# Kernel optimization log

Hardware: AMD Instinct MI355X
Metric: run time of the kernel (lower is better)

## Reference

```python
import jax, jax.numpy as jnp
import numpy as np

N, E = 20000, 160000
F, H, OUT = 256, 8, 128
L = 6            # total layers -> 5 GAT layers
LM1 = L - 1
NGN = L // 3 + 1 # 3 GraphNorms
D = F // H       # 32 per head
GN_FREQ = 3
EPS = 1e-5


def setup_inputs() -> dict:
    key = jax.random.key(0)
    ks = jax.random.split(key, 12)
    x = jax.random.normal(ks[0], (N, 1), dtype=jnp.float32)
    edge_index = jax.random.randint(ks[1], (2, E), 0, N, dtype=jnp.int32)
    W0 = jax.random.normal(ks[2], (1, F), dtype=jnp.float32) * 0.1
    b0 = jnp.zeros((F,), jnp.float32)
    gat_lin = jax.random.normal(ks[3], (LM1, F, F), dtype=jnp.float32) * (1.0 / np.sqrt(F))
    att_src = jax.random.normal(ks[4], (LM1, H, D), dtype=jnp.float32) * 0.1
    att_dst = jax.random.normal(ks[5], (LM1, H, D), dtype=jnp.float32) * 0.1
    gat_bias = jnp.zeros((LM1, F), jnp.float32)
    gn_weight = jnp.ones((NGN, F), jnp.float32)
    gn_bias = jnp.zeros((NGN, F), jnp.float32)
    gn_mean_scale = jnp.ones((NGN, F), jnp.float32)
    lin_W = jax.random.normal(ks[6], (F, OUT), dtype=jnp.float32) * (1.0 / np.sqrt(F))
    lin_b = jnp.zeros((OUT,), jnp.float32)
    return {"x": x, "W0": W0, "b0": b0, "gat_lin": gat_lin, "att_src": att_src,
            "att_dst": att_dst, "gat_bias": gat_bias, "gn_weight": gn_weight,
            "gn_bias": gn_bias, "gn_mean_scale": gn_mean_scale,
            "lin_W": lin_W, "lin_b": lin_b, "edge_index": edge_index}


def _gcn_conv(x, W, b, src, dst, n):
    h = x @ W
    deg = jax.ops.segment_sum(jnp.ones(src.shape[0], h.dtype), dst, num_segments=n)
    dinv = jnp.where(deg > 0, jax.lax.rsqrt(deg), 0.0)
    norm = dinv[src] * dinv[dst]                      # [E']
    out = jax.ops.segment_sum(h[src] * norm[:, None], dst, num_segments=n)
    return out + b


def _gat_conv(x, W, a_src, a_dst, src, dst, n):
    # PyG GATConv (concat=True, negative_slope=0.2, self-loops in src/dst)
    h = (x @ W).reshape(n, H, D)
    s = jnp.einsum('nhd,hd->nh', h, a_src)            # [N,H]
    t = jnp.einsum('nhd,hd->nh', h, a_dst)
    e = jax.nn.leaky_relu(s[src] + t[dst], 0.2)       # [E',H]
    m = jax.ops.segment_max(e, dst, num_segments=n)   # per-dst softmax
    e = jnp.exp(e - m[dst])
    denom = jax.ops.segment_sum(e, dst, num_segments=n)
    alpha = e / (denom[dst] + 1e-16)
    out = jax.ops.segment_sum(h[src] * alpha[:, :, None], dst, num_segments=n)
    return out.reshape(n, F)


def _graph_norm(x, w, b, ms):
    # PyG GraphNorm with batch=None (single graph): per-feature stats over nodes
    mean = jnp.mean(x, axis=0)
    out = x - ms * mean
    var = jnp.mean(out * out, axis=0)
    return w * out * jax.lax.rsqrt(var + EPS) + b


def reference(x, W0, b0, gat_lin, att_src, att_dst, gat_bias, gn_weight, gn_bias,
              gn_mean_scale, lin_W, lin_b, edge_index):
    n = x.shape[0]
    loops = jnp.arange(n, dtype=edge_index.dtype)
    src = jnp.concatenate([edge_index[0], loops])
    dst = jnp.concatenate([edge_index[1], loops])
    h = jax.nn.relu(_gcn_conv(x, W0, b0, src, dst, n))
    for i in range(LM1):
        if i % GN_FREQ == 0:
            g = i // GN_FREQ
            h = _graph_norm(h, gn_weight[g], gn_bias[g], gn_mean_scale[g])
        out = _gat_conv(h, gat_lin[i], att_src[i], att_dst[i], src, dst, n)
        if i % GN_FREQ == 0:
            out = out + gat_bias[i]
        h = h + jax.nn.relu(out)
    return h @ lin_W + lin_b
```

## Files before the change

### kernel.cpp

```cpp
#include <hip/hip_runtime.h>
#include <hip/hip_bf16.h>
#include <stdint.h>

typedef float f32x4 __attribute__((ext_vector_type(4)));
typedef short s16x8 __attribute__((ext_vector_type(8)));

__device__ __forceinline__ float bf2f(unsigned short u) {
    union { unsigned int i; float f; } v; v.i = ((unsigned int)u) << 16; return v.f;
}
__device__ __forceinline__ unsigned short f2bf(float f) {
    union { float f; unsigned int i; } v; v.f = f;
    unsigned int x = v.i;
    return (unsigned short)((x + 0x7fffu + ((x >> 16) & 1u)) >> 16);
}
__device__ __forceinline__ void gload16(const void* g, void* l) {
    __builtin_amdgcn_global_load_lds(
        (const __attribute__((address_space(1))) void*)g,
        (__attribute__((address_space(3))) void*)l, 16, 0, 0);
}

__global__ void k_init_deg(int* deg, int n) {
    int i = blockIdx.x * blockDim.x + threadIdx.x;
    if (i < n) deg[i] = 1;
}

__global__ void k_count(const int* __restrict__ ei, int E, int* deg) {
    int e = blockIdx.x * blockDim.x + threadIdx.x;
    if (e < E) atomicAdd(&deg[ei[E + e]], 1);
}

__global__ __launch_bounds__(256) void k_bsum(const int* __restrict__ deg,
                                              int* __restrict__ bsum, int n) {
    __shared__ int buf[256];
    int i = blockIdx.x * 256 + threadIdx.x;
    buf[threadIdx.x] = (i < n) ? deg[i] : 0;
    __syncthreads();
#pragma unroll
    for (int off = 128; off > 0; off >>= 1) {
        if ((int)threadIdx.x < off) buf[threadIdx.x] += buf[threadIdx.x + off];
        __syncthreads();
    }
    if (threadIdx.x == 0) bsum[blockIdx.x] = buf[0];
}

__global__ __launch_bounds__(256) void k_scanb(const int* __restrict__ bsum,
                                               int* __restrict__ boff, int nb) {
    __shared__ int buf[256];
    int t = threadIdx.x;
    int v = (t < nb) ? bsum[t] : 0;
    buf[t] = v;
    __syncthreads();
    for (int off = 1; off < 256; off <<= 1) {
        int add = (t >= off) ? buf[t - off] : 0;
        __syncthreads();
        buf[t] += add;
        __syncthreads();
    }
    if (t < nb) boff[t] = buf[t] - v;
}

__global__ __launch_bounds__(256) void k_emit(const int* __restrict__ deg,
                                              const int* __restrict__ boff,
                                              int* __restrict__ rowptr,
                                              int* __restrict__ wo,
                                              float* __restrict__ dinv, int n) {
    __shared__ int buf[256];
    int i = blockIdx.x * 256 + threadIdx.x;
    int v = (i < n) ? deg[i] : 0;
    buf[threadIdx.x] = v;
    __syncthreads();
    for (int off = 1; off < 256; off <<= 1) {
        int add = ((int)threadIdx.x >= off) ? buf[threadIdx.x - off] : 0;
        __syncthreads();
        buf[threadIdx.x] += add;
        __syncthreads();
    }
    if (i < n) {
        int excl = boff[blockIdx.x] + buf[threadIdx.x] - v;
        rowptr[i] = excl;
        wo[i] = excl;
        dinv[i] = rsqrtf((float)v);
        if (i == n - 1) rowptr[n] = excl + v;
    }
}

__global__ void k_fill(const int* __restrict__ ei, int E, int n,
                       int* wo, int* srcs) {
    int e = blockIdx.x * blockDim.x + threadIdx.x;
    int EP = E + n;
    if (e >= EP) return;
    int s_, d_;
    if (e < E) { s_ = ei[e]; d_ = ei[E + e]; }
    else       { s_ = d_ = e - E; }
    int pos = atomicAdd(&wo[d_], 1);
    srcs[pos] = s_;
}

__global__ __launch_bounds__(256) void k_h0f(const float* __restrict__ x,
                                             const float* __restrict__ dinv,
                                             const int* __restrict__ rowptr,
                                             const int* __restrict__ srcs,
                                             const float* __restrict__ W0,
                                             const float* __restrict__ b0,
                                             unsigned short* __restrict__ hbf, int n) {
    int node = blockIdx.x;
    int tid = threadIdx.x;
    if (node >= n) { hbf[(size_t)node * 256 + tid] = 0; return; }
    __shared__ float sv;
    if (tid < 64) {
        int p0 = rowptr[node], p1 = rowptr[node + 1];
        float sum = 0.f;
        for (int p = p0 + tid; p < p1; p += 64) {
            int s = srcs[p];
            sum += x[s] * dinv[s];
        }
#pragma unroll
        for (int m = 1; m < 64; m <<= 1) sum += __shfl_xor(sum, m);
        if (tid == 0) sv = sum * dinv[node];
    }
    __syncthreads();
    float v = fmaxf(sv * W0[tid] + b0[tid], 0.f);
    hbf[(size_t)node * 256 + tid] = f2bf(v);
}

__global__ void k_wprep(const float* __restrict__ gat_lin,
                        const float* __restrict__ lin_W,
                        const float* __restrict__ att_src,
                        const float* __restrict__ att_dst,
                        unsigned short* __restrict__ Wt,
                        unsigned short* __restrict__ lt) {
    int idx = blockIdx.x * blockDim.x + threadIdx.x;
    const int T1 = 5 * 65536;
    const int T2 = T1 + 128 * 256;
    const int T3 = T2 + 5 * 64 * 256;
    if (idx < T1) {
        int l = idx >> 16, r = idx & 0xFFFF;
        int nrow = r >> 8, k = r & 255;
        Wt[(size_t)l * 81920 + nrow * 256 + k] =
            f2bf(gat_lin[(size_t)l * 65536 + k * 256 + nrow]);
    } else if (idx < T2) {
        int j = idx - T1;
        int nrow = j >> 8, k = j & 255;
        lt[nrow * 256 + k] = f2bf(lin_W[(size_t)k * 128 + nrow]);
    } else if (idx < T3) {
        int j = idx - T2;
        int l = j >> 14, r = j & 16383;
        int row = r >> 8, k = r & 255;
        float v = 0.f;
        if (row < 16) {
            int head = row & 7;
            const float* a = (row < 8) ? (att_src + l * 256 + head * 32)
                                       : (att_dst + l * 256 + head * 32);
            const float* wr = gat_lin + (size_t)l * 65536 + k * 256 + head * 32;
#pragma unroll
            for (int d = 0; d < 32; ++d) v += wr[d] * a[d];
        }
        Wt[(size_t)l * 81920 + (256 + row) * 256 + k] = f2bf(v);
    }
}

__global__ __launch_bounds__(256) void k_gn_reduce(const unsigned short* __restrict__ hbf,
                                                   float* sums, float* sumsq, int n) {
    int f = threadIdx.x;
    float s = 0.f, q = 0.f;
    for (int r = blockIdx.x; r < n; r += gridDim.x) {
        float v = bf2f(hbf[(size_t)r * 256 + f]);
        s += v; q += v * v;
    }
    atomicAdd(&sums[f], s);
    atomicAdd(&sumsq[f], q);
}

__global__ void k_gn_apply(unsigned short* __restrict__ hbf,
                           const float* __restrict__ stats,
                           const float* __restrict__ w, const float* __restrict__ b,
                           const float* __restrict__ ms, float ninv) {
    int node = blockIdx.x, f = threadIdx.x;
    float mean = stats[f] * ninv;
    float m2   = stats[256 + f] * ninv;
    float msf  = ms[f];
    float var  = m2 + msf * mean * mean * (msf - 2.0f);
    float scale = w[f] * rsqrtf(var + 1e-5f);
    size_t idx = (size_t)node * 256 + f;
    float v = (bf2f(hbf[idx]) - msf * mean) * scale + b[f];
    hbf[idx] = f2bf(v);
}

#define BM 64
__global__ __launch_bounds__(512) void k_gemm_mfma(
    const unsigned short* __restrict__ A,
    const unsigned short* __restrict__ Bt,
    unsigned short* __restrict__ Cb,
    float* __restrict__ Cf,
    float* __restrict__ sbuf,
    float* __restrict__ tbuf,
    const float* __restrict__ bias,
    int M, int ldc, int nbTot, int nbPerY)
{
    __shared__ unsigned short As[64 * 256];
    __shared__ unsigned short Bs[2][64 * 256];
    const int tid = threadIdx.x;
    const int bm = blockIdx.x * BM;
    const int nb0 = blockIdx.y * nbPerY;
    int nb1 = nb0 + nbPerY; if (nb1 > nbTot) nb1 = nbTot;

    {
        const char* ga = (const char*)(A + (size_t)bm * 256);
        const char* gb = (const char*)(Bt + (size_t)nb0 * 16384);
        char* la = (char*)As;
        char* lb = (char*)Bs[0];
#pragma unroll
        for (int i = 0; i < 4; ++i) {
            int o  = (i * 512 + tid) * 16;
            int so = o ^ (((o >> 9) & 7) << 4);
            gload16(ga + so, la + o);
            gload16(gb + so, lb + o);
        }
    }
    __syncthreads();

    const int lane = tid & 63;
    const int w  = tid >> 6;
    const int wm = (w >> 1) * 16;
    const int wn = (w & 1) * 32;
    const int r  = lane & 15, kb = lane >> 4;
    const int r4 = (lane >> 4) * 4, cc = lane & 15;
    const char* la = (const char*)As;

    for (int nb = nb0; nb < nb1; ++nb) {
        int cur = (nb - nb0) & 1;
        if (nb + 1 < nb1) {
            const char* gb = (const char*)(Bt + (size_t)(nb + 1) * 16384);
            char* lb = (char*)Bs[cur ^ 1];
#pragma unroll
            for (int i = 0; i < 4; ++i) {
                int o  = (i * 512 + tid) * 16;
                int so = o ^ (((o >> 9) & 7) << 4);
                gload16(gb + so, lb + o);
            }
        }
        const char* lb = (const char*)Bs[cur];
        f32x4 acc[2] = {};
#pragma unroll
        for (int ks = 0; ks < 8; ++ks) {
            int row = wm + r;
            int c16 = (ks * 4 + kb) ^ (row & 7);
            s16x8 af = *(const s16x8*)(la + row * 512 + c16 * 16);
#pragma unroll
            for (int j = 0; j < 2; ++j) {
                int col = wn + j * 16 + r;
                int d16 = (ks * 4 + kb) ^ (col & 7);
                s16x8 bfr = *(const s16x8*)(lb + col * 512 + d16 * 16);
                acc[j] = __builtin_amdgcn_mfma_f32_16x16x32_bf16(af, bfr, acc[j], 0, 0, 0);
            }
        }
#pragma unroll
        for (int j = 0; j < 2; ++j) {
            int col = nb * 64 + wn + j * 16 + cc;
#pragma unroll
            for (int q = 0; q < 4; ++q) {
                int row = bm + wm + r4 + q;
                float v = acc[j][q];
                if (Cb) {
                    if (col < 256) {
                        Cb[(size_t)row * 256 + col] = f2bf(v);
                    } else if (col < 264) {
                        sbuf[(size_t)row * 8 + (col - 256)] = v;
                    } else if (col < 272) {
                        tbuf[(size_t)row * 8 + (col - 264)] = v;
                    }
                } else if (row < M) {
                    Cf[(size_t)row * ldc + col] = v + bias[col];
                }
            }
        }
        __syncthreads();
    }
}

__global__ __launch_bounds__(256) void k_fagg(const unsigned short* __restrict__ h1,
                                              const float* __restrict__ sbuf,
                                              const float* __restrict__ tbuf,
                                              const int* __restrict__ rowptr,
                                              const int* __restrict__ srcs,
                                              unsigned short* __restrict__ hbf,
                                              const float* __restrict__ bias, int n) {
    int wave = threadIdx.x >> 6, lane = threadIdx.x & 63;
    int node = blockIdx.x * 4 + wave;
    if (node >= n) return;
    int p0 = rowptr[node], p1 = rowptr[node + 1];
    int head = lane >> 3;
    float tv = tbuf[node * 8 + head];
    float m = -1e30f;
    int p = p0;
    for (; p + 3 < p1; p += 4) {
        float e0 = sbuf[srcs[p]     * 8 + head];
        float e1 = sbuf[srcs[p + 1] * 8 + head];
        float e2 = sbuf[srcs[p + 2] * 8 + head];
        float e3 = sbuf[srcs[p + 3] * 8 + head];
        m = fmaxf(m, fmaxf(fmaxf(e0, e1), fmaxf(e2, e3)));
    }
    for (; p < p1; ++p) m = fmaxf(m, sbuf[srcs[p] * 8 + head]);
    m += tv;
    m = (m > 0.f) ? m : 0.2f * m;
    float den = 1e-16f;
    float a0 = 0.f, a1 = 0.f, a2 = 0.f, a3 = 0.f;
    float c0 = 0.f, c1 = 0.f, c2 = 0.f, c3 = 0.f;
    float d0 = 0.f, d1 = 0.f, d2 = 0.f, d3 = 0.f;
    float g0 = 0.f, g1 = 0.f, g2 = 0.f, g3 = 0.f;
    p = p0;
    for (; p + 3 < p1; p += 4) {
        int s0 = srcs[p], s1 = srcs[p + 1], s2 = srcs[p + 2], s3 = srcs[p + 3];
        float e0 = sbuf[s0 * 8 + head] + tv;
        float e1 = sbuf[s1 * 8 + head] + tv;
        float e2 = sbuf[s2 * 8 + head] + tv;
        float e3 = sbuf[s3 * 8 + head] + tv;
        e0 = (e0 > 0.f) ? e0 : 0.2f * e0;
        e1 = (e1 > 0.f) ? e1 : 0.2f * e1;
        e2 = (e2 > 0.f) ? e2 : 0.2f * e2;
        e3 = (e3 > 0.f) ? e3 : 0.2f * e3;
        float w0 = __expf(e0 - m), w1 = __expf(e1 - m);
        float w2 = __expf(e2 - m), w3 = __expf(e3 - m);
        ushort4 v0 = reinterpret_cast<const ushort4*>(h1 + (size_t)s0 * 256)[lane];
        ushort4 v1 = reinterpret_cast<const ushort4*>(h1 + (size_t)s1 * 256)[lane];
        ushort4 v2 = reinterpret_cast<const ushort4*>(h1 + (size_t)s2 * 256)[lane];
        ushort4 v3 = reinterpret_cast<const ushort4*>(h1 + (size_t)s3 * 256)[lane];
        den += (w0 + w1) + (w2 + w3);
        a0 += w0 * bf2f(v0.x); a1 += w0 * bf2f(v0.y);
        a2 += w0 * bf2f(v0.z); a3 += w0 * bf2f(v0.w);
        c0 += w1 * bf2f(v1.x); c1 += w1 * bf2f(v1.y);
        c2 += w1 * bf2f(v1.z); c3 += w1 * bf2f(v1.w);
        d0 += w2 * bf2f(v2.x); d1 += w2 * bf2f(v2.y);
        d2 += w2 * bf2f(v2.z); d3 += w2 * bf2f(v2.w);
        g0 += w3 * bf2f(v3.x); g1 += w3 * bf2f(v3.y);
        g2 += w3 * bf2f(v3.z); g3 += w3 * bf2f(v3.w);
    }
    for (; p < p1; ++p) {
        int s0 = srcs[p];
        float e0 = sbuf[s0 * 8 + head] + tv;
        e0 = (e0 > 0.f) ? e0 : 0.2f * e0;
        float w0 = __expf(e0 - m);
        ushort4 v0 = reinterpret_cast<const ushort4*>(h1 + (size_t)s0 * 256)[lane];
        den += w0;
        a0 += w0 * bf2f(v0.x); a1 += w0 * bf2f(v0.y);
        a2 += w0 * bf2f(v0.z); a3 += w0 * bf2f(v0.w);
    }
    float inv = 1.0f / den;
    a0 = ((a0 + c0) + (d0 + g0)) * inv;
    a1 = ((a1 + c1) + (d1 + g1)) * inv;
    a2 = ((a2 + c2) + (d2 + g2)) * inv;
    a3 = ((a3 + c3) + (d3 + g3)) * inv;
    float b0_ = 0.f, b1_ = 0.f, b2_ = 0.f, b3_ = 0.f;
    if (bias) {
        float4 bb = reinterpret_cast<const float4*>(bias)[lane];
        b0_ = bb.x; b1_ = bb.y; b2_ = bb.z; b3_ = bb.w;
    }
    size_t base = (size_t)node * 256 + lane * 4;
    ushort4 hv = *reinterpret_cast<const ushort4*>(hbf + base);
    ushort4 o;
    o.x = f2bf(bf2f(hv.x) + fmaxf(a0 + b0_, 0.f));
    o.y = f2bf(bf2f(hv.y) + fmaxf(a1 + b1_, 0.f));
    o.z = f2bf(bf2f(hv.z) + fmaxf(a2 + b2_, 0.f));
    o.w = f2bf(bf2f(hv.w) + fmaxf(a3 + b3_, 0.f));
    *reinterpret_cast<ushort4*>(hbf + base) = o;
}

extern "C" void kernel_launch(void* const* d_in, const int* in_sizes, int n_in,
                              void* d_out, int out_size, void* d_ws, size_t ws_size,
                              hipStream_t stream) {
    const float* x        = (const float*)d_in[0];
    const float* W0       = (const float*)d_in[1];
    const float* b0       = (const float*)d_in[2];
    const float* gat_lin  = (const float*)d_in[3];
    const float* att_src  = (const float*)d_in[4];
    const float* att_dst  = (const float*)d_in[5];
    const float* gat_bias = (const float*)d_in[6];
    const float* gn_w     = (const float*)d_in[7];
    const float* gn_b     = (const float*)d_in[8];
    const float* gn_ms    = (const float*)d_in[9];
    const float* lin_W    = (const float*)d_in[10];
    const float* lin_b    = (const float*)d_in[11];
    const int*   ei       = (const int*)d_in[12];

    const int n  = in_sizes[0];
    const int E  = in_sizes[12] / 2;
    const int EP = E + n;
    const int Mpad = ((n + BM - 1) / BM) * BM;
    const int nb = (n + 255) / 256;

    char* w = (char*)d_ws;
    unsigned short* hbf = (unsigned short*)w; w += (size_t)Mpad * 256 * 2;
    unsigned short* h1  = (unsigned short*)w; w += (size_t)Mpad * 256 * 2;
    float* sbuf = (float*)w;                  w += (size_t)Mpad * 8 * 4;
    float* tbuf = (float*)w;                  w += (size_t)Mpad * 8 * 4;
    unsigned short* Wt = (unsigned short*)w;  w += (size_t)5 * 320 * 256 * 2;
    unsigned short* lt = (unsigned short*)w;  w += (size_t)128 * 256 * 2;
    float* gnstat = (float*)w;                w += 1024 * 4;
    float* dinv = (float*)w;                  w += (size_t)n * 4;
    int* deg    = (int*)w;                    w += (size_t)n * 4;
    int* rowptr = (int*)w;                    w += ((size_t)(n + 1) * 4 + 15) / 16 * 16;
    int* wo     = (int*)w;                    w += (size_t)n * 4;
    int* bsum   = (int*)w;                    w += ((size_t)nb * 4 + 15) / 16 * 16;
    int* boff   = (int*)w;                    w += ((size_t)nb * 4 + 15) / 16 * 16;
    int* srcs   = (int*)w;                    w += (size_t)EP * 4;

    const int B256 = 256;
    auto cdiv = [](int a, int b) { return (a + b - 1) / b; };

    hipMemsetAsync(gnstat, 0, 1024 * 4, stream);

    const int WPREP = 5 * 65536 + 128 * 256 + 5 * 64 * 256;
    k_wprep<<<cdiv(WPREP, B256), B256, 0, stream>>>(gat_lin, lin_W, att_src, att_dst, Wt, lt);

    k_init_deg<<<cdiv(n, B256), B256, 0, stream>>>(deg, n);
    k_count<<<cdiv(E, B256), B256, 0, stream>>>(ei, E, deg);
    k_bsum<<<nb, 256, 0, stream>>>(deg, bsum, n);
    k_scanb<<<1, 256, 0, stream>>>(bsum, boff, nb);
    k_emit<<<nb, 256, 0, stream>>>(deg, boff, rowptr, wo, dinv, n);
    k_fill<<<cdiv(EP, B256), B256, 0, stream>>>(ei, E, n, wo, srcs);

    k_h0f<<<Mpad, 256, 0, stream>>>(x, dinv, rowptr, srcs, W0, b0, hbf, n);

    const float ninv = 1.0f / (float)n;
    const int gx = Mpad / BM;

    for (int i = 0; i < 5; ++i) {
        if (i % 3 == 0) {
            int g = i / 3;
            k_gn_reduce<<<256, 256, 0, stream>>>(hbf, gnstat + g * 512,
                                                 gnstat + g * 512 + 256, n);
            k_gn_apply<<<n, 256, 0, stream>>>(hbf, gnstat + g * 512,
                                              gn_w + g * 256, gn_b + g * 256,
                                              gn_ms + g * 256, ninv);
        }
        k_gemm_mfma<<<dim3(gx, 2), 512, 0, stream>>>(
            hbf, Wt + (size_t)i * 81920, h1, nullptr, sbuf, tbuf, nullptr, n, 256, 5, 3);
        k_fagg<<<cdiv(n, 4), 256, 0, stream>>>(
            h1, sbuf, tbuf, rowptr, srcs, hbf,
            (i % 3 == 0) ? gat_bias + i * 256 : nullptr, n);
    }

    k_gemm_mfma<<<dim3(gx, 1), 512, 0, stream>>>(
        hbf, lt, nullptr, (float*)d_out, nullptr, nullptr, lin_b, n, 128, 2, 2);
}
```

Baseline: 350.0 us.

## Fold GraphNorm into GEMM weights, use online softmax in aggregation, merge init kernels

GraphNorm is no longer a separate pass over the node features. Its per-feature scale is folded into the transposed GAT weights, its offset becomes a per-column bias added in the GEMM epilogue, and the residual path applies scale and offset inside the aggregation kernel. The aggregation kernel switches from two passes (max, then weighted sum) to a single online-softmax pass, which avoids re-reading the source indices and attention scores. Degree initialisation is merged into the memset with the self-loop +1 added at read time, and the first GCN layer uses one wave per node instead of one block. The trade-offs are extra exp/rescale work per edge chunk and the folded weights being quantised to bf16 after scaling, which may shift numerics slightly.

```diff
diff --git a/kernel.cpp b/kernel.cpp
--- a/kernel.cpp
+++ b/kernel.cpp
@@ -19,11 +19,6 @@
         (__attribute__((address_space(3))) void*)l, 16, 0, 0);
 }
 
-__global__ void k_init_deg(int* deg, int n) {
-    int i = blockIdx.x * blockDim.x + threadIdx.x;
-    if (i < n) deg[i] = 1;
-}
-
 __global__ void k_count(const int* __restrict__ ei, int E, int* deg) {
     int e = blockIdx.x * blockDim.x + threadIdx.x;
     if (e < E) atomicAdd(&deg[ei[E + e]], 1);
@@ -33,7 +28,7 @@
                                               int* __restrict__ bsum, int n) {
     __shared__ int buf[256];
     int i = blockIdx.x * 256 + threadIdx.x;
-    buf[threadIdx.x] = (i < n) ? deg[i] : 0;
+    buf[threadIdx.x] = (i < n) ? deg[i] + 1 : 0;
     __syncthreads();
 #pragma unroll
     for (int off = 128; off > 0; off >>= 1) {
@@ -66,7 +61,7 @@
                                               float* __restrict__ dinv, int n) {
     __shared__ int buf[256];
     int i = blockIdx.x * 256 + threadIdx.x;
-    int v = (i < n) ? deg[i] : 0;
+    int v = (i < n) ? deg[i] + 1 : 0;
     buf[threadIdx.x] = v;
     __syncthreads();
     for (int off = 1; off < 256; off <<= 1) {
@@ -102,25 +97,34 @@
                                              const int* __restrict__ srcs,
                                              const float* __restrict__ W0,
                                              const float* __restrict__ b0,
-                                             unsigned short* __restrict__ hbf, int n) {
-    int node = blockIdx.x;
-    int tid = threadIdx.x;
-    if (node >= n) { hbf[(size_t)node * 256 + tid] = 0; return; }
-    __shared__ float sv;
-    if (tid < 64) {
-        int p0 = rowptr[node], p1 = rowptr[node + 1];
-        float sum = 0.f;
-        for (int p = p0 + tid; p < p1; p += 64) {
-            int s = srcs[p];
-            sum += x[s] * dinv[s];
-        }
-#pragma unroll
-        for (int m = 1; m < 64; m <<= 1) sum += __shfl_xor(sum, m);
-        if (tid == 0) sv = sum * dinv[node];
-    }
-    __syncthreads();
-    float v = fmaxf(sv * W0[tid] + b0[tid], 0.f);
-    hbf[(size_t)node * 256 + tid] = f2bf(v);
+                                             unsigned short* __restrict__ hbf,
+                                             int n, int Mpad) {
+    int wave = threadIdx.x >> 6, lane = threadIdx.x & 63;
+    int node = blockIdx.x * 4 + wave;
+    if (node >= Mpad) return;
+    size_t base = (size_t)node * 256 + lane * 4;
+    if (node >= n) {
+        ushort4 z = {0, 0, 0, 0};
+        *reinterpret_cast<ushort4*>(hbf + base) = z;
+        return;
+    }
+    int p0 = rowptr[node], p1 = rowptr[node + 1];
+    float sum = 0.f;
+    for (int p = p0 + lane; p < p1; p += 64) {
+        int s = srcs[p];
+        sum += x[s] * dinv[s];
+    }
+#pragma unroll
+    for (int m = 1; m < 64; m <<= 1) sum += __shfl_xor(sum, m);
+    float sv = sum * dinv[node];
+    float4 wv = *reinterpret_cast<const float4*>(W0 + lane * 4);
+    float4 bv = *reinterpret_cast<const float4*>(b0 + lane * 4);
+    ushort4 o;
+    o.x = f2bf(fmaxf(sv * wv.x + bv.x, 0.f));
+    o.y = f2bf(fmaxf(sv * wv.y + bv.y, 0.f));
+    o.z = f2bf(fmaxf(sv * wv.z + bv.z, 0.f));
+    o.w = f2bf(fmaxf(sv * wv.w + bv.w, 0.f));
+    *reinterpret_cast<ushort4*>(hbf + base) = o;
 }
 
 __global__ void k_wprep(const float* __restrict__ gat_lin,
@@ -171,19 +175,34 @@
     atomicAdd(&sumsq[f], q);
 }
 
-__global__ void k_gn_apply(unsigned short* __restrict__ hbf,
-                           const float* __restrict__ stats,
-                           const float* __restrict__ w, const float* __restrict__ b,
-                           const float* __restrict__ ms, float ninv) {
-    int node = blockIdx.x, f = threadIdx.x;
-    float mean = stats[f] * ninv;
-    float m2   = stats[256 + f] * ninv;
-    float msf  = ms[f];
+__global__ __launch_bounds__(256) void k_gnfold(const float* __restrict__ st,
+                                                const float* __restrict__ w,
+                                                const float* __restrict__ b,
+                                                const float* __restrict__ ms,
+                                                unsigned short* __restrict__ Wt,
+                                                float* __restrict__ so,
+                                                float* __restrict__ rowbias,
+                                                float ninv) {
+    __shared__ float red[256];
+    int col = blockIdx.x, k = threadIdx.x;
+    float mean = st[k] * ninv;
+    float m2   = st[256 + k] * ninv;
+    float msf  = ms[k];
     float var  = m2 + msf * mean * mean * (msf - 2.0f);
-    float scale = w[f] * rsqrtf(var + 1e-5f);
-    size_t idx = (size_t)node * 256 + f;
-    float v = (bf2f(hbf[idx]) - msf * mean) * scale + b[f];
-    hbf[idx] = f2bf(v);
+    float sc = w[k] * rsqrtf(var + 1e-5f);
+    float of = b[k] - msf * mean * sc;
+    size_t idx = (size_t)col * 256 + k;
+    float wv = bf2f(Wt[idx]);
+    red[k] = of * wv;
+    __syncthreads();
+#pragma unroll
+    for (int off = 128; off > 0; off >>= 1) {
+        if (k < off) red[k] += red[k + off];
+        __syncthreads();
+    }
+    if (k == 0) rowbias[col] = red[0];
+    Wt[idx] = f2bf(sc * wv);
+    if (col == 0) { so[k] = sc; so[256 + k] = of; }
 }
 
 #define BM 64
@@ -195,6 +214,7 @@
     float* __restrict__ sbuf,
     float* __restrict__ tbuf,
     const float* __restrict__ bias,
+    const float* __restrict__ rowbias,
     int M, int ldc, int nbTot, int nbPerY)
 {
     __shared__ unsigned short As[64 * 256];
@@ -257,10 +277,11 @@
 #pragma unroll
         for (int j = 0; j < 2; ++j) {
             int col = nb * 64 + wn + j * 16 + cc;
+            float rb = rowbias ? rowbias[col] : 0.f;
 #pragma unroll
             for (int q = 0; q < 4; ++q) {
                 int row = bm + wm + r4 + q;
-                float v = acc[j][q];
+                float v = acc[j][q] + rb;
                 if (Cb) {
                     if (col < 256) {
                         Cb[(size_t)row * 256 + col] = f2bf(v);
@@ -284,72 +305,60 @@
                                               const int* __restrict__ rowptr,
                                               const int* __restrict__ srcs,
                                               unsigned short* __restrict__ hbf,
-                                              const float* __restrict__ bias, int n) {
+                                              const float* __restrict__ bias,
+                                              const float* __restrict__ so, int n) {
     int wave = threadIdx.x >> 6, lane = threadIdx.x & 63;
     int node = blockIdx.x * 4 + wave;
     if (node >= n) return;
     int p0 = rowptr[node], p1 = rowptr[node + 1];
     int head = lane >> 3;
     float tv = tbuf[node * 8 + head];
-    float m = -1e30f;
+    float m = -1e30f, den = 0.f;
+    float a0 = 0.f, a1 = 0.f, a2 = 0.f, a3 = 0.f;
     int p = p0;
-    for (; p + 3 < p1; p += 4) {
-        float e0 = sbuf[srcs[p]     * 8 + head];
-        float e1 = sbuf[srcs[p + 1] * 8 + head];
-        float e2 = sbuf[srcs[p + 2] * 8 + head];
-        float e3 = sbuf[srcs[p + 3] * 8 + head];
-        m = fmaxf(m, fmaxf(fmaxf(e0, e1), fmaxf(e2, e3)));
-    }
-    for (; p < p1; ++p) m = fmaxf(m, sbuf[srcs[p] * 8 + head]);
-    m += tv;
-    m = (m > 0.f) ? m : 0.2f * m;
-    float den = 1e-16f;
-    float a0 = 0.f, a1 = 0.f, a2 = 0.f, a3 = 0.f;
-    float c0 = 0.f, c1 = 0.f, c2 = 0.f, c3 = 0.f;
-    float d0 = 0.f, d1 = 0.f, d2 = 0.f, d3 = 0.f;
-    float g0 = 0.f, g1 = 0.f, g2 = 0.f, g3 = 0.f;
-    p = p0;
     for (; p + 3 < p1; p += 4) {
         int s0 = srcs[p], s1 = srcs[p + 1], s2 = srcs[p + 2], s3 = srcs[p + 3];
         float e0 = sbuf[s0 * 8 + head] + tv;
         float e1 = sbuf[s1 * 8 + head] + tv;
         float e2 = sbuf[s2 * 8 + head] + tv;
         float e3 = sbuf[s3 * 8 + head] + tv;
+        ushort4 v0 = reinterpret_cast<const ushort4*>(h1 + (size_t)s0 * 256)[lane];
+        ushort4 v1 = reinterpret_cast<const ushort4*>(h1 + (size_t)s1 * 256)[lane];
+        ushort4 v2 = reinterpret_cast<const ushort4*>(h1 + (size_t)s2 * 256)[lane];
+        ushort4 v3 = reinterpret_cast<const ushort4*>(h1 + (size_t)s3 * 256)[lane];
         e0 = (e0 > 0.f) ? e0 : 0.2f * e0;
         e1 = (e1 > 0.f) ? e1 : 0.2f * e1;
         e2 = (e2 > 0.f) ? e2 : 0.2f * e2;
         e3 = (e3 > 0.f) ? e3 : 0.2f * e3;
-        float w0 = __expf(e0 - m), w1 = __expf(e1 - m);
-        float w2 = __expf(e2 - m), w3 = __expf(e3 - m);
-        ushort4 v0 = reinterpret_cast<const ushort4*>(h1 + (size_t)s0 * 256)[lane];
-        ushort4 v1 = reinterpret_cast<const ushort4*>(h1 + (size_t)s1 * 256)[lane];
-        ushort4 v2 = reinterpret_cast<const ushort4*>(h1 + (size_t)s2 * 256)[lane];
-        ushort4 v3 = reinterpret_cast<const ushort4*>(h1 + (size_t)s3 * 256)[lane];
-        den += (w0 + w1) + (w2 + w3);
-        a0 += w0 * bf2f(v0.x); a1 += w0 * bf2f(v0.y);
-        a2 += w0 * bf2f(v0.z); a3 += w0 * bf2f(v0.w);
-        c0 += w1 * bf2f(v1.x); c1 += w1 * bf2f(v1.y);
-        c2 += w1 * bf2f(v1.z); c3 += w1 * bf2f(v1.w);
-        d0 += w2 * bf2f(v2.x); d1 += w2 * bf2f(v2.y);
-        d2 += w2 * bf2f(v2.z); d3 += w2 * bf2f(v2.w);
-        g0 += w3 * bf2f(v3.x); g1 += w3 * bf2f(v3.y);
-        g2 += w3 * bf2f(v3.z); g3 += w3 * bf2f(v3.w);
+        float em = fmaxf(fmaxf(e0, e1), fmaxf(e2, e3));
+        float mn = fmaxf(m, em);
+        float sc = __expf(m - mn);
+        float w0 = __expf(e0 - mn), w1 = __expf(e1 - mn);
+        float w2 = __expf(e2 - mn), w3 = __expf(e3 - mn);
+        den = den * sc + ((w0 + w1) + (w2 + w3));
+        a0 = fmaf(a0, sc, w0 * bf2f(v0.x) + w1 * bf2f(v1.x) + w2 * bf2f(v2.x) + w3 * bf2f(v3.x));
+        a1 = fmaf(a1, sc, w0 * bf2f(v0.y) + w1 * bf2f(v1.y) + w2 * bf2f(v2.y) + w3 * bf2f(v3.y));
+        a2 = fmaf(a2, sc, w0 * bf2f(v0.z) + w1 * bf2f(v1.z) + w2 * bf2f(v2.z) + w3 * bf2f(v3.z));
+        a3 = fmaf(a3, sc, w0 * bf2f(v0.w) + w1 * bf2f(v1.w) + w2 * bf2f(v2.w) + w3 * bf2f(v3.w));
+        m = mn;
     }
     for (; p < p1; ++p) {
         int s0 = srcs[p];
         float e0 = sbuf[s0 * 8 + head] + tv;
         e0 = (e0 > 0.f) ? e0 : 0.2f * e0;
-        float w0 = __expf(e0 - m);
         ushort4 v0 = reinterpret_cast<const ushort4*>(h1 + (size_t)s0 * 256)[lane];
-        den += w0;
-        a0 += w0 * bf2f(v0.x); a1 += w0 * bf2f(v0.y);
-        a2 += w0 * bf2f(v0.z); a3 += w0 * bf2f(v0.w);
-    }
-    float inv = 1.0f / den;
-    a0 = ((a0 + c0) + (d0 + g0)) * inv;
-    a1 = ((a1 + c1) + (d1 + g1)) * inv;
-    a2 = ((a2 + c2) + (d2 + g2)) * inv;
-    a3 = ((a3 + c3) + (d3 + g3)) * inv;
+        float mn = fmaxf(m, e0);
+        float sc = __expf(m - mn);
+        float w0 = __expf(e0 - mn);
+        den = den * sc + w0;
+        a0 = fmaf(a0, sc, w0 * bf2f(v0.x));
+        a1 = fmaf(a1, sc, w0 * bf2f(v0.y));
+        a2 = fmaf(a2, sc, w0 * bf2f(v0.z));
+        a3 = fmaf(a3, sc, w0 * bf2f(v0.w));
+        m = mn;
+    }
+    float inv = 1.0f / (den + 1e-16f);
+    a0 *= inv; a1 *= inv; a2 *= inv; a3 *= inv;
     float b0_ = 0.f, b1_ = 0.f, b2_ = 0.f, b3_ = 0.f;
     if (bias) {
         float4 bb = reinterpret_cast<const float4*>(bias)[lane];
@@ -357,11 +366,18 @@
     }
     size_t base = (size_t)node * 256 + lane * 4;
     ushort4 hv = *reinterpret_cast<const ushort4*>(hbf + base);
+    float h0 = bf2f(hv.x), h1v = bf2f(hv.y), h2 = bf2f(hv.z), h3 = bf2f(hv.w);
+    if (so) {
+        float4 sc4 = reinterpret_cast<const float4*>(so)[lane];
+        float4 of4 = reinterpret_cast<const float4*>(so + 256)[lane];
+        h0 = h0 * sc4.x + of4.x; h1v = h1v * sc4.y + of4.y;
+        h2 = h2 * sc4.z + of4.z; h3 = h3 * sc4.w + of4.w;
+    }
     ushort4 o;
-    o.x = f2bf(bf2f(hv.x) + fmaxf(a0 + b0_, 0.f));
-    o.y = f2bf(bf2f(hv.y) + fmaxf(a1 + b1_, 0.f));
-    o.z = f2bf(bf2f(hv.z) + fmaxf(a2 + b2_, 0.f));
-    o.w = f2bf(bf2f(hv.w) + fmaxf(a3 + b3_, 0.f));
+    o.x = f2bf(h0  + fmaxf(a0 + b0_, 0.f));
+    o.y = f2bf(h1v + fmaxf(a1 + b1_, 0.f));
+    o.z = f2bf(h2  + fmaxf(a2 + b2_, 0.f));
+    o.w = f2bf(h3  + fmaxf(a3 + b3_, 0.f));
     *reinterpret_cast<ushort4*>(hbf + base) = o;
 }
 
@@ -395,9 +411,11 @@
     float* tbuf = (float*)w;                  w += (size_t)Mpad * 8 * 4;
     unsigned short* Wt = (unsigned short*)w;  w += (size_t)5 * 320 * 256 * 2;
     unsigned short* lt = (unsigned short*)w;  w += (size_t)128 * 256 * 2;
+    float* scaleoff = (float*)w;              w += 1024 * 4;
+    float* rowbias  = (float*)w;              w += 640 * 4;
     float* gnstat = (float*)w;                w += 1024 * 4;
+    int* deg    = (int*)w;                    w += (size_t)n * 4;
     float* dinv = (float*)w;                  w += (size_t)n * 4;
-    int* deg    = (int*)w;                    w += (size_t)n * 4;
     int* rowptr = (int*)w;                    w += ((size_t)(n + 1) * 4 + 15) / 16 * 16;
     int* wo     = (int*)w;                    w += (size_t)n * 4;
     int* bsum   = (int*)w;                    w += ((size_t)nb * 4 + 15) / 16 * 16;
@@ -407,39 +425,45 @@
     const int B256 = 256;
     auto cdiv = [](int a, int b) { return (a + b - 1) / b; };
 
-    hipMemsetAsync(gnstat, 0, 1024 * 4, stream);
+    hipMemsetAsync(gnstat, 0, 1024 * 4 + (size_t)n * 4, stream);
 
     const int WPREP = 5 * 65536 + 128 * 256 + 5 * 64 * 256;
     k_wprep<<<cdiv(WPREP, B256), B256, 0, stream>>>(gat_lin, lin_W, att_src, att_dst, Wt, lt);
 
-    k_init_deg<<<cdiv(n, B256), B256, 0, stream>>>(deg, n);
     k_count<<<cdiv(E, B256), B256, 0, stream>>>(ei, E, deg);
     k_bsum<<<nb, 256, 0, stream>>>(deg, bsum, n);
     k_scanb<<<1, 256, 0, stream>>>(bsum, boff, nb);
     k_emit<<<nb, 256, 0, stream>>>(deg, boff, rowptr, wo, dinv, n);
     k_fill<<<cdiv(EP, B256), B256, 0, stream>>>(ei, E, n, wo, srcs);
 
-    k_h0f<<<Mpad, 256, 0, stream>>>(x, dinv, rowptr, srcs, W0, b0, hbf, n);
+    k_h0f<<<cdiv(Mpad, 4), 256, 0, stream>>>(x, dinv, rowptr, srcs, W0, b0, hbf, n, Mpad);
 
     const float ninv = 1.0f / (float)n;
     const int gx = Mpad / BM;
 
     for (int i = 0; i < 5; ++i) {
+        const float* rb = nullptr;
+        const float* so = nullptr;
         if (i % 3 == 0) {
             int g = i / 3;
             k_gn_reduce<<<256, 256, 0, stream>>>(hbf, gnstat + g * 512,
                                                  gnstat + g * 512 + 256, n);
-            k_gn_apply<<<n, 256, 0, stream>>>(hbf, gnstat + g * 512,
-                                              gn_w + g * 256, gn_b + g * 256,
-                                              gn_ms + g * 256, ninv);
+            k_gnfold<<<320, 256, 0, stream>>>(gnstat + g * 512, gn_w + g * 256,
+                                              gn_b + g * 256, gn_ms + g * 256,
+                                              Wt + (size_t)i * 81920,
+                                              scaleoff + g * 512, rowbias + g * 320, ninv);
+            rb = rowbias + g * 320;
+            so = scaleoff + g * 512;
         }
         k_gemm_mfma<<<dim3(gx, 2), 512, 0, stream>>>(
-            hbf, Wt + (size_t)i * 81920, h1, nullptr, sbuf, tbuf, nullptr, n, 256, 5, 3);
+            hbf, Wt + (size_t)i * 81920, h1, nullptr, sbuf, tbuf, nullptr, rb,
+            n, 256, 5, 3);
         k_fagg<<<cdiv(n, 4), 256, 0, stream>>>(
             h1, sbuf, tbuf, rowptr, srcs, hbf,
-            (i % 3 == 0) ? gat_bias + i * 256 : nullptr, n);
+            (i % 3 == 0) ? gat_bias + i * 256 : nullptr, so, n);
     }
 
     k_gemm_mfma<<<dim3(gx, 1), 512, 0, stream>>>(
-        hbf, lt, nullptr, (float*)d_out, nullptr, nullptr, lin_b, n, 128, 2, 2);
-}
+        hbf, lt, nullptr, (float*)d_out, nullptr, nullptr, lin_b, nullptr,
+        n, 128, 2, 2);
+}
```

Result: faster. 309.1 us (-11.7%).
